# Kernel optimization log

Hardware: AMD Instinct MI355X
Metric: run time of the kernel (lower is better)

The kernel has to match this reference:

```python
import jax, jax.numpy as jnp
import numpy as np

# NOTE: ffn(in, out, capacity=1, activation) is assumed to be a single Linear(in, out)
# followed by the activation (ReLU). Dropout is identity in eval mode.

B, M, H, Eh = 16, 128, 256, 128

def setup_inputs() -> dict:
    key = jax.random.key(0)
    ks = jax.random.split(key, 12)
    s = lambda n: 1.0 / np.sqrt(n)
    return {
        "X": jax.random.normal(ks[0], (B, M, H), jnp.float32),
        "E": jax.random.normal(ks[1], (B, M, M, Eh), jnp.float32),
        "A": jax.random.uniform(ks[2], (B, M, M), jnp.float32),
        "eps": jnp.zeros((1,), jnp.float32),
        "We": jax.random.normal(ks[3], (Eh, Eh), jnp.float32) * s(Eh),
        "be": jnp.zeros((Eh,), jnp.float32),
        "Wr": jax.random.normal(ks[4], (H + Eh, H), jnp.float32) * s(H + Eh),
        "br": jnp.zeros((H,), jnp.float32),
        "W0": jax.random.normal(ks[5], (H, H), jnp.float32) * s(H),
        "b0": jnp.zeros((H,), jnp.float32),
        "W1": jax.random.normal(ks[6], (H, H), jnp.float32) * s(H),
        "b1": jnp.zeros((H,), jnp.float32),
    }

def reference(X, E, A, eps, We, be, Wr, br, W0, b0, W1, b1):
    act = jax.nn.relu
    # edge_mapper: ffn(e, e, capacity=1) -> Linear + activation
    Em = act(jnp.einsum('bije,ef->bijf', E, We) + be)          # (b,m,m,e)
    # msg[b,j,:] = sum_i A[b,i,j] * cat(X[b,i,:], Em[b,i,j,:])
    # fused: avoids materializing the (b,m,m,h+e) intermediate
    msg_x = jnp.einsum('bij,bih->bjh', A, X)                   # (b,m,h)
    msg_e = jnp.einsum('bij,bije->bje', A, Em)                 # (b,m,e)
    msg = jnp.concatenate([msg_x, msg_e], axis=-1)             # (b,m,h+e)
    Xs = (1.0 + eps) * X
    out = Xs + act(jnp.einsum('bmc,ch->bmh', msg, Wr) + br)    # residual_mapping
    out = jnp.einsum('bmh,hk->bmk', out, W0) + b0
    out = act(out)  # dropout p is identity in eval mode
    out = jnp.einsum('bmh,hk->bmk', out, W1) + b1
    out = act(out)
    return out
```

## Files before the change

### kernel.cpp

```cpp
#include <hip/hip_runtime.h>

typedef float        f32x4  __attribute__((ext_vector_type(4)));
typedef __bf16       bf16x8 __attribute__((ext_vector_type(8)));
typedef unsigned int u32x4  __attribute__((ext_vector_type(4)));
typedef unsigned short u16;

#define MFMA16(a,b,c) __builtin_amdgcn_mfma_f32_16x16x32_bf16((a),(b),(c),0,0,0)

typedef __attribute__((address_space(3))) unsigned int       as3_u32;
typedef __attribute__((address_space(1))) const unsigned int as1_u32;
__device__ __forceinline__ void gld16(const float* g, float* l) {
    __builtin_amdgcn_global_load_lds((as1_u32*)g, (as3_u32*)l, 16, 0, 0);
}

__device__ __forceinline__ unsigned bf_rnd(float x) {
    unsigned u = __float_as_uint(x);
    return (u + 0x7FFFu + ((u >> 16) & 1u)) & 0xFFFF0000u;
}
__device__ __forceinline__ void split_bf(float x, unsigned &h, unsigned &l) {
    unsigned hr = bf_rnd(x);
    h = hr >> 16;
    float lo = x - __uint_as_float(hr);
    l = bf_rnd(lo) >> 16;
}
__device__ __forceinline__ void split8q(const f32x4 a, const f32x4 b, bf16x8 &hv, bf16x8 &lv) {
    u32x4 hp, lp;
    #pragma unroll
    for (int i = 0; i < 2; ++i) {
        float x0 = (i ? b : a)[0], x1 = (i ? b : a)[1], x2 = (i ? b : a)[2], x3 = (i ? b : a)[3];
        unsigned h0 = __float_as_uint(x0) & 0xFFFF0000u;
        unsigned h1 = __float_as_uint(x1) & 0xFFFF0000u;
        unsigned h2 = __float_as_uint(x2) & 0xFFFF0000u;
        unsigned h3 = __float_as_uint(x3) & 0xFFFF0000u;
        unsigned l0 = bf_rnd(x0 - __uint_as_float(h0));
        unsigned l1 = bf_rnd(x1 - __uint_as_float(h1));
        unsigned l2 = bf_rnd(x2 - __uint_as_float(h2));
        unsigned l3 = bf_rnd(x3 - __uint_as_float(h3));
        hp[i*2+0] = (h0 >> 16) | h1;  lp[i*2+0] = (l0 >> 16) | l1;
        hp[i*2+1] = (h2 >> 16) | h3;  lp[i*2+1] = (l2 >> 16) | l3;
    }
    hv = __builtin_bit_cast(bf16x8, hp);
    lv = __builtin_bit_cast(bf16x8, lp);
}
__device__ __forceinline__ bf16x8 ld16(const u16* p) {
    return __builtin_bit_cast(bf16x8, *(const u32x4*)p);
}

__global__ __launch_bounds__(256) void k_prep(
    const float* __restrict__ We, const float* __restrict__ Wr,
    const float* __restrict__ W0, const float* __restrict__ W1,
    u16* __restrict__ WeTh, u16* __restrict__ WeTl,
    u16* __restrict__ WrTh, u16* __restrict__ WrTl,
    u16* __restrict__ W0Th, u16* __restrict__ W0Tl,
    u16* __restrict__ W1Th, u16* __restrict__ W1Tl)
{
    int t = blockIdx.x * 256 + threadIdx.x;
    float v; u16 *dh, *dl; int dst;
    if (t < 16384) {
        int f = t & 127, e = t >> 7;
        v = We[e*128 + f];
        int F = ((f>>6)*4 + ((f>>4)&3))*4 + (e>>5);
        dst = F*512 + (((e>>3)&3)*16 + (f&15))*8 + (e&7);
        dh = WeTh; dl = WeTl;
    } else if (t < 114688) {
        int u = t - 16384; int h = u & 255, k = u >> 8;
        v = Wr[k*256 + h];
        int F = (h>>4)*12 + (k>>5);
        dst = F*512 + (((k>>3)&3)*16 + (h&15))*8 + (k&7);
        dh = WrTh; dl = WrTl;
    } else if (t < 180224) {
        int u = t - 114688; int h = u & 255, k = u >> 8;
        v = W0[k*256 + h];
        int F = (h>>4)*8 + (k>>5);
        dst = F*512 + (((k>>3)&3)*16 + (h&15))*8 + (k&7);
        dh = W0Th; dl = W0Tl;
    } else {
        int u = t - 180224; int h = u & 255, k = u >> 8;
        v = W1[k*256 + h];
        int F = (h>>4)*8 + (k>>5);
        dst = F*512 + (((k>>3)&3)*16 + (h&15))*8 + (k&7);
        dh = W1Th; dl = W1Tl;
    }
    unsigned hh, ll; split_bf(v, hh, ll);
    dh[dst] = (u16)hh; dl[dst] = (u16)ll;
}

__device__ __forceinline__ void stage_slab(const float* __restrict__ Eslab,
                                           float* buf, int tid) {
    const int w = tid >> 6, l = tid & 63;
    #pragma unroll
    for (int r = 0; r < 4; ++r) {
        const int q   = (r << 2) + w;
        const int row = (q << 1) + (l >> 5);
        const int c   = ((l & 31) ^ (row & 7)) << 2;
        gld16(Eslab + row*128 + c, buf + (q << 8));
    }
}

__global__ __launch_bounds__(256) __attribute__((amdgpu_waves_per_eu(2, 2)))
void k_edge(
    const float* __restrict__ E, const float* __restrict__ A,
    const u16* __restrict__ WeTh, const u16* __restrict__ WeTl,
    const float* __restrict__ be, float* __restrict__ part)
{
    __shared__ __align__(16) float sEf[4*4096];
    __shared__ __align__(16) float sA[512];

    const int tid  = threadIdx.x;
    const int lane = tid & 63;
    const int wv   = tid >> 6;
    const int lrow = lane & 15;
    const int lk   = lane >> 4;
    const int wm   = (wv >> 1) << 4;
    const int wn   = (wv & 1)  << 6;
    const int bid  = blockIdx.x;
    const int jh   = bid & 3;
    const int c    = (bid >> 2) & 7;
    const int b    = bid >> 5;
    const int i0   = c << 4;
    const int j0   = jh << 5;

    #pragma unroll
    for (int q = 0; q < 2; ++q) {
        const int idx = q*256 + tid;
        sA[idx] = A[(size_t)(b*128 + i0 + (idx >> 5))*128 + j0 + (idx & 31)];
    }
    float ber[4];
    #pragma unroll
    for (int n = 0; n < 4; ++n) ber[n] = be[wn + n*16 + lrow];

    bf16x8 wh[4][4], wl[4][4];
    {
        const int F0 = (wv & 1) * 16;
        #pragma unroll
        for (int n = 0; n < 4; ++n)
            #pragma unroll
            for (int k = 0; k < 4; ++k) {
                const int off = (F0 + n*4 + k)*512 + lane*8;
                wh[n][k] = ld16(WeTh + off);
                wl[n][k] = ld16(WeTl + off);
            }
    }
    asm volatile("s_waitcnt vmcnt(0) lgkmcnt(0)" ::: "memory");

    const float* Eb = E + ((size_t)((b*128 + i0)*128 + j0)) * 128;
    stage_slab(Eb,            sEf,          tid);
    stage_slab(Eb + 16384,    sEf + 4096,   tid);
    stage_slab(Eb + 2*16384,  sEf + 2*4096, tid);

    f32x4 P[4] = {};

#define EDGE_STEP(S, NWs)                                                    \
    {                                                                        \
        asm volatile("s_waitcnt vmcnt(" NWs ")" ::: "memory");               \
        __builtin_amdgcn_s_barrier();                                        \
        __builtin_amdgcn_sched_barrier(0);                                   \
        if ((S) < 13)                                                        \
            stage_slab(Eb + (size_t)((S)+3)*16384,                           \
                       sEf + (((S)+3) & 3)*4096, tid);                       \
        const char* buf = (const char*)(sEf + ((S) & 3)*4096);               \
        const int jr = wm + lrow;                                            \
        const int sw = (jr & 7) << 4;                                        \
        f32x4 em[4] = {};                                                    \
        _Pragma("unroll")                                                    \
        for (int k = 0; k < 4; ++k) {                                        \
            const int cb = k*128 + lk*32;                                    \
            const f32x4 e0 = *(const f32x4*)(buf + jr*512 + ((cb +  0)^sw)); \
            const f32x4 e1 = *(const f32x4*)(buf + jr*512 + ((cb + 16)^sw)); \
            bf16x8 eh, el; split8q(e0, e1, eh, el);                          \
            _Pragma("unroll")                                                \
            for (int n = 0; n < 4; ++n) {                                    \
                em[n] = MFMA16(eh, wh[n][k], em[n]);                         \
                em[n] = MFMA16(eh, wl[n][k], em[n]);                         \
                em[n] = MFMA16(el, wh[n][k], em[n]);                         \
            }                                                                \
        }                                                                    \
        const f32x4 a4 = *(const f32x4*)(sA + (S)*32 + wm + lk*4);           \
        _Pragma("unroll")                                                    \
        for (int n = 0; n < 4; ++n)                                          \
            _Pragma("unroll")                                                \
            for (int r = 0; r < 4; ++r) {                                    \
                float v = fmaxf(em[n][r] + ber[n], 0.0f);                    \
                P[n][r] += a4[r] * v;                                        \
            }                                                                \
    }

    EDGE_STEP(0,  "8")  EDGE_STEP(1,  "8")  EDGE_STEP(2,  "8")
    EDGE_STEP(3,  "8")  EDGE_STEP(4,  "8")  EDGE_STEP(5,  "8")
    EDGE_STEP(6,  "8")  EDGE_STEP(7,  "8")  EDGE_STEP(8,  "8")
    EDGE_STEP(9,  "8")  EDGE_STEP(10, "8")  EDGE_STEP(11, "8")
    EDGE_STEP(12, "8")  EDGE_STEP(13, "8")  EDGE_STEP(14, "4")
    EDGE_STEP(15, "0")
#undef EDGE_STEP

    float* op = part + (size_t)bid * 4096;
    #pragma unroll
    for (int r = 0; r < 4; ++r) {
        const int j = wm + lk*4 + r;
        #pragma unroll
        for (int n = 0; n < 4; ++n)
            op[j*128 + wn + n*16 + lrow] = P[n][r];
    }
}

__global__ __launch_bounds__(256) void k_msg(
    const float* __restrict__ A, const float* __restrict__ X,
    const float* __restrict__ part,
    u16* __restrict__ msg_h, u16* __restrict__ msg_l)
{
    const int bid = blockIdx.x;
    const int tid = threadIdx.x;
    __shared__ float sAt[128*8];

    if (bid < 256) {
        const int b = bid >> 4, jt = bid & 15;
        #pragma unroll
        for (int q = 0; q < 4; ++q) {
            const int e   = (q << 8) + tid;
            const int row = jt*8 + (e >> 7);
            const int f   = e & 127;
            const float* p = part + ((size_t)b*32 + (row >> 5))*4096
                                  + (row & 31)*128 + f;
            float ssum = 0.f;
            #pragma unroll
            for (int cc = 0; cc < 8; ++cc) ssum += p[(size_t)cc*16384];
            unsigned hh, ll; split_bf(ssum, hh, ll);
            const size_t o = (size_t)(b*128 + row)*384 + 256 + f;
            msg_h[o] = (u16)hh; msg_l[o] = (u16)ll;
        }
    } else {
        const int idx = bid - 256;
        const int b = idx >> 4, jt = idx & 15, j0 = jt << 3;
        #pragma unroll
        for (int q = 0; q < 4; ++q) {
            const int e = tid + q*256;
            sAt[e] = A[(size_t)(b*128 + (e >> 3))*128 + j0 + (e & 7)];
        }
        __syncthreads();
        const int h = tid;
        float acc[8] = {};
        const float* Xb = X + (size_t)b*32768 + h;
        #pragma unroll 2
        for (int i = 0; i < 128; ++i) {
            const float x  = Xb[(size_t)i*256];
            const f32x4 a0 = *(const f32x4*)(sAt + i*8);
            const f32x4 a1 = *(const f32x4*)(sAt + i*8 + 4);
            acc[0] += a0[0]*x; acc[1] += a0[1]*x; acc[2] += a0[2]*x; acc[3] += a0[3]*x;
            acc[4] += a1[0]*x; acc[5] += a1[1]*x; acc[6] += a1[2]*x; acc[7] += a1[3]*x;
        }
        #pragma unroll
        for (int jj = 0; jj < 8; ++jj) {
            unsigned hh, ll; split_bf(acc[jj], hh, ll);
            const size_t o = (size_t)(b*128 + j0 + jj)*384 + h;
            msg_h[o] = (u16)hh; msg_l[o] = (u16)ll;
        }
    }
}

template<int KT, bool RES, bool F32OUT>
__global__ __launch_bounds__(256) void k_tail(
    const u16* __restrict__ Ah, const u16* __restrict__ Al,
    const u16* __restrict__ Bh, const u16* __restrict__ Bl,
    const float* __restrict__ bias, const float* __restrict__ res,
    const float* __restrict__ epsp,
    float* __restrict__ outf, u16* __restrict__ oh, u16* __restrict__ ol)
{
    constexpr int NB = KT/32;
    const int tid  = threadIdx.x;
    const int lane = tid & 63;
    const int wid  = tid >> 6;
    const int lrow = lane & 15;
    const int lk   = lane >> 4;
    const int wm   = (wid >> 1) << 4;
    const int wn   = (wid & 1)  << 5;
    const int r0   = blockIdx.x << 5;
    const int h0   = blockIdx.y << 6;

    const int arow = r0 + wm + lrow;
    const u16* pah = Ah + (size_t)arow*KT + lk*8;
    const u16* pal = Al + (size_t)arow*KT + lk*8;
    const size_t bb = (size_t)((h0 + wn) >> 4) * NB * 512 + lane*8;
    const u16* pbh = Bh + bb;
    const u16* pbl = Bl + bb;

    f32x4 P[2] = {};
    #pragma unroll
    for (int ks = 0; ks < NB; ++ks) {
        const bf16x8 ah  = ld16(pah + ks*32);
        const bf16x8 al  = ld16(pal + ks*32);
        const bf16x8 b0h = ld16(pbh + ks*512), b0l = ld16(pbl + ks*512);
        const bf16x8 b1h = ld16(pbh + (NB + ks)*512), b1l = ld16(pbl + (NB + ks)*512);
        P[0] = MFMA16(ah, b0h, P[0]);
        P[0] = MFMA16(ah, b0l, P[0]);
        P[0] = MFMA16(al, b0h, P[0]);
        P[1] = MFMA16(ah, b1h, P[1]);
        P[1] = MFMA16(ah, b1l, P[1]);
        P[1] = MFMA16(al, b1h, P[1]);
    }

    const float eps = RES ? epsp[0] : 0.f;
    #pragma unroll
    for (int n = 0; n < 2; ++n) {
        const int col = h0 + wn + n*16 + lrow;
        const float bv = bias[col];
        #pragma unroll
        for (int e = 0; e < 4; ++e) {
            const int r = r0 + wm + lk*4 + e;
            float v = fmaxf(P[n][e] + bv, 0.f);
            if (RES) v += (1.f + eps) * res[(size_t)r*256 + col];
            if (F32OUT) {
                outf[(size_t)r*256 + col] = v;
            } else {
                unsigned hh, ll; split_bf(v, hh, ll);
                oh[(size_t)r*256 + col] = (u16)hh;
                ol[(size_t)r*256 + col] = (u16)ll;
            }
        }
    }
}

extern "C" void kernel_launch(void* const* d_in, const int* in_sizes, int n_in,
                              void* d_out, int out_size, void* d_ws, size_t ws_size,
                              hipStream_t stream)
{
    const float* X   = (const float*)d_in[0];
    const float* E   = (const float*)d_in[1];
    const float* A   = (const float*)d_in[2];
    const float* eps = (const float*)d_in[3];
    const float* We  = (const float*)d_in[4];
    const float* be  = (const float*)d_in[5];
    const float* Wr  = (const float*)d_in[6];
    const float* br  = (const float*)d_in[7];
    const float* W0  = (const float*)d_in[8];
    const float* b0  = (const float*)d_in[9];
    const float* W1  = (const float*)d_in[10];
    const float* b1  = (const float*)d_in[11];
    float* out = (float*)d_out;

    u16* w = (u16*)d_ws;
    u16* WeTh = w;              u16* WeTl = WeTh + 16384;
    u16* WrTh = WeTl + 16384;   u16* WrTl = WrTh + 98304;
    u16* W0Th = WrTl + 98304;   u16* W0Tl = W0Th + 65536;
    u16* W1Th = W0Tl + 65536;   u16* W1Tl = W1Th + 65536;
    u16* msg_h = W1Tl + 65536;  u16* msg_l = msg_h + 786432;
    u16* o1h = msg_l + 786432;  u16* o1l = o1h + 524288;
    u16* o2h = o1l + 524288;    u16* o2l = o2h + 524288;
    float* part = (float*)(o2l + 524288);

    k_prep<<<960, 256, 0, stream>>>(We, Wr, W0, W1,
        WeTh, WeTl, WrTh, WrTl, W0Th, W0Tl, W1Th, W1Tl);
    k_edge<<<512, 256, 0, stream>>>(E, A, WeTh, WeTl, be, part);
    k_msg<<<512, 256, 0, stream>>>(A, X, part, msg_h, msg_l);
    k_tail<384, true , false><<<dim3(64,4), 256, 0, stream>>>(
        msg_h, msg_l, WrTh, WrTl, br, X, eps, nullptr, o1h, o1l);
    k_tail<256, false, false><<<dim3(64,4), 256, 0, stream>>>(
        o1h, o1l, W0Th, W0Tl, b0, nullptr, nullptr, nullptr, o2h, o2l);
    k_tail<256, false, true ><<<dim3(64,4), 256, 0, stream>>>(
        o2h, o2l, W1Th, W1Tl, b1, nullptr, nullptr, out, nullptr, nullptr);
}
```

Baseline: 267.4 us.

## Load edge tiles directly into registers with double buffering, drop LDS staging

The edge kernel no longer stages E slabs through LDS using global_load_lds with barriers. Each lane now loads its own E fragments and A values straight into registers, double-buffered across steps. The block grows to 512 threads with 8 waves, each covering 32 output features, and the grid halves so each block handles 32 i-rows instead of 16. The We prep layout and the partial reduction in k_msg change to match. The aim is to remove LDS traffic and barrier stalls, at the cost of uncoalesced per-lane global loads and higher register pressure.

```diff
diff --git a/kernel.cpp b/kernel.cpp
--- a/kernel.cpp
+++ b/kernel.cpp
@@ -6,12 +6,6 @@
 typedef unsigned short u16;
 
 #define MFMA16(a,b,c) __builtin_amdgcn_mfma_f32_16x16x32_bf16((a),(b),(c),0,0,0)
-
-typedef __attribute__((address_space(3))) unsigned int       as3_u32;
-typedef __attribute__((address_space(1))) const unsigned int as1_u32;
-__device__ __forceinline__ void gld16(const float* g, float* l) {
-    __builtin_amdgcn_global_load_lds((as1_u32*)g, (as3_u32*)l, 16, 0, 0);
-}
 
 __device__ __forceinline__ unsigned bf_rnd(float x) {
     unsigned u = __float_as_uint(x);
@@ -59,7 +53,7 @@
     if (t < 16384) {
         int f = t & 127, e = t >> 7;
         v = We[e*128 + f];
-        int F = ((f>>6)*4 + ((f>>4)&3))*4 + (e>>5);
+        int F = (f>>4)*4 + (e>>5);
         dst = F*512 + (((e>>3)&3)*16 + (f&15))*8 + (e&7);
         dh = WeTh; dl = WeTl;
     } else if (t < 114688) {
@@ -85,120 +79,96 @@
     dh[dst] = (u16)hh; dl[dst] = (u16)ll;
 }
 
-__device__ __forceinline__ void stage_slab(const float* __restrict__ Eslab,
-                                           float* buf, int tid) {
-    const int w = tid >> 6, l = tid & 63;
-    #pragma unroll
-    for (int r = 0; r < 4; ++r) {
-        const int q   = (r << 2) + w;
-        const int row = (q << 1) + (l >> 5);
-        const int c   = ((l & 31) ^ (row & 7)) << 2;
-        gld16(Eslab + row*128 + c, buf + (q << 8));
-    }
-}
-
-__global__ __launch_bounds__(256) __attribute__((amdgpu_waves_per_eu(2, 2)))
+__global__ __launch_bounds__(512) __attribute__((amdgpu_waves_per_eu(2, 2)))
 void k_edge(
     const float* __restrict__ E, const float* __restrict__ A,
     const u16* __restrict__ WeTh, const u16* __restrict__ WeTl,
     const float* __restrict__ be, float* __restrict__ part)
 {
-    __shared__ __align__(16) float sEf[4*4096];
-    __shared__ __align__(16) float sA[512];
-
     const int tid  = threadIdx.x;
     const int lane = tid & 63;
     const int wv   = tid >> 6;
     const int lrow = lane & 15;
     const int lk   = lane >> 4;
-    const int wm   = (wv >> 1) << 4;
-    const int wn   = (wv & 1)  << 6;
+    const int jg   = wv >> 2;
+    const int fg   = wv & 3;
+    const int wm   = jg << 4;
+    const int wn   = fg << 5;
     const int bid  = blockIdx.x;
-    const int jh   = bid & 3;
-    const int c    = (bid >> 2) & 7;
-    const int b    = bid >> 5;
-    const int i0   = c << 4;
+    const int c    = bid & 3;
+    const int jh   = (bid >> 2) & 3;
+    const int b    = bid >> 4;
+    const int i0   = c << 5;
     const int j0   = jh << 5;
 
-    #pragma unroll
-    for (int q = 0; q < 2; ++q) {
-        const int idx = q*256 + tid;
-        sA[idx] = A[(size_t)(b*128 + i0 + (idx >> 5))*128 + j0 + (idx & 31)];
-    }
-    float ber[4];
-    #pragma unroll
-    for (int n = 0; n < 4; ++n) ber[n] = be[wn + n*16 + lrow];
-
-    bf16x8 wh[4][4], wl[4][4];
-    {
-        const int F0 = (wv & 1) * 16;
-        #pragma unroll
-        for (int n = 0; n < 4; ++n)
-            #pragma unroll
-            for (int k = 0; k < 4; ++k) {
-                const int off = (F0 + n*4 + k)*512 + lane*8;
-                wh[n][k] = ld16(WeTh + off);
-                wl[n][k] = ld16(WeTl + off);
-            }
-    }
-    asm volatile("s_waitcnt vmcnt(0) lgkmcnt(0)" ::: "memory");
-
-    const float* Eb = E + ((size_t)((b*128 + i0)*128 + j0)) * 128;
-    stage_slab(Eb,            sEf,          tid);
-    stage_slab(Eb + 16384,    sEf + 4096,   tid);
-    stage_slab(Eb + 2*16384,  sEf + 2*4096, tid);
-
-    f32x4 P[4] = {};
-
-#define EDGE_STEP(S, NWs)                                                    \
-    {                                                                        \
-        asm volatile("s_waitcnt vmcnt(" NWs ")" ::: "memory");               \
-        __builtin_amdgcn_s_barrier();                                        \
-        __builtin_amdgcn_sched_barrier(0);                                   \
-        if ((S) < 13)                                                        \
-            stage_slab(Eb + (size_t)((S)+3)*16384,                           \
-                       sEf + (((S)+3) & 3)*4096, tid);                       \
-        const char* buf = (const char*)(sEf + ((S) & 3)*4096);               \
-        const int jr = wm + lrow;                                            \
-        const int sw = (jr & 7) << 4;                                        \
-        f32x4 em[4] = {};                                                    \
-        _Pragma("unroll")                                                    \
-        for (int k = 0; k < 4; ++k) {                                        \
-            const int cb = k*128 + lk*32;                                    \
-            const f32x4 e0 = *(const f32x4*)(buf + jr*512 + ((cb +  0)^sw)); \
-            const f32x4 e1 = *(const f32x4*)(buf + jr*512 + ((cb + 16)^sw)); \
-            bf16x8 eh, el; split8q(e0, e1, eh, el);                          \
-            _Pragma("unroll")                                                \
-            for (int n = 0; n < 4; ++n) {                                    \
-                em[n] = MFMA16(eh, wh[n][k], em[n]);                         \
-                em[n] = MFMA16(eh, wl[n][k], em[n]);                         \
-                em[n] = MFMA16(el, wh[n][k], em[n]);                         \
-            }                                                                \
-        }                                                                    \
-        const f32x4 a4 = *(const f32x4*)(sA + (S)*32 + wm + lk*4);           \
-        _Pragma("unroll")                                                    \
-        for (int n = 0; n < 4; ++n)                                          \
-            _Pragma("unroll")                                                \
-            for (int r = 0; r < 4; ++r) {                                    \
-                float v = fmaxf(em[n][r] + ber[n], 0.0f);                    \
-                P[n][r] += a4[r] * v;                                        \
-            }                                                                \
-    }
-
-    EDGE_STEP(0,  "8")  EDGE_STEP(1,  "8")  EDGE_STEP(2,  "8")
-    EDGE_STEP(3,  "8")  EDGE_STEP(4,  "8")  EDGE_STEP(5,  "8")
-    EDGE_STEP(6,  "8")  EDGE_STEP(7,  "8")  EDGE_STEP(8,  "8")
-    EDGE_STEP(9,  "8")  EDGE_STEP(10, "8")  EDGE_STEP(11, "8")
-    EDGE_STEP(12, "8")  EDGE_STEP(13, "8")  EDGE_STEP(14, "4")
-    EDGE_STEP(15, "0")
-#undef EDGE_STEP
+    bf16x8 wh[2][4], wl[2][4];
+    #pragma unroll
+    for (int n = 0; n < 2; ++n)
+        #pragma unroll
+        for (int k = 0; k < 4; ++k) {
+            const int off = (((fg*2 + n)*4) + k)*512 + lane*8;
+            wh[n][k] = ld16(WeTh + off);
+            wl[n][k] = ld16(WeTl + off);
+        }
+    float ber[2];
+    #pragma unroll
+    for (int n = 0; n < 2; ++n) ber[n] = be[wn + n*16 + lrow];
+
+    const float* Erow = E + ((size_t)(b*128 + i0)*128 + j0 + wm + lrow)*128 + lk*8;
+    const float* Arow = A + ((size_t)(b*128 + i0))*128 + j0 + wm + lk*4;
+
+#define LOADSLAB(dst, adst, s)                                          \
+    {                                                                   \
+        const float* p = Erow + (size_t)(s)*16384;                      \
+        _Pragma("unroll")                                               \
+        for (int k = 0; k < 4; ++k) {                                   \
+            dst[k*2+0] = *(const f32x4*)(p + k*32);                     \
+            dst[k*2+1] = *(const f32x4*)(p + k*32 + 4);                 \
+        }                                                               \
+        adst = *(const f32x4*)(Arow + (size_t)(s)*128);                 \
+    }
+
+    f32x4 ebA[8], ebB[8], a4A, a4B;
+    LOADSLAB(ebA, a4A, 0)
+
+    f32x4 P[2] = {};
+
+#define STEP(EBC, AC, EBN, AN, s)                                       \
+    {                                                                   \
+        if ((s) < 31) LOADSLAB(EBN, AN, (s)+1)                          \
+        f32x4 em0 = {}, em1 = {};                                       \
+        _Pragma("unroll")                                               \
+        for (int k = 0; k < 4; ++k) {                                   \
+            bf16x8 eh, el; split8q(EBC[k*2], EBC[k*2+1], eh, el);       \
+            em0 = MFMA16(eh, wh[0][k], em0);                            \
+            em0 = MFMA16(eh, wl[0][k], em0);                            \
+            em0 = MFMA16(el, wh[0][k], em0);                            \
+            em1 = MFMA16(eh, wh[1][k], em1);                            \
+            em1 = MFMA16(eh, wl[1][k], em1);                            \
+            em1 = MFMA16(el, wh[1][k], em1);                            \
+        }                                                               \
+        _Pragma("unroll")                                               \
+        for (int r = 0; r < 4; ++r) {                                   \
+            float v0 = fmaxf(em0[r] + ber[0], 0.0f);                    \
+            float v1 = fmaxf(em1[r] + ber[1], 0.0f);                    \
+            P[0][r] += AC[r] * v0;                                      \
+            P[1][r] += AC[r] * v1;                                      \
+        }                                                               \
+    }
+
+    for (int s = 0; s < 32; s += 2) {
+        STEP(ebA, a4A, ebB, a4B, s)
+        STEP(ebB, a4B, ebA, a4A, s+1)
+    }
+#undef STEP
+#undef LOADSLAB
 
     float* op = part + (size_t)bid * 4096;
     #pragma unroll
     for (int r = 0; r < 4; ++r) {
         const int j = wm + lk*4 + r;
         #pragma unroll
-        for (int n = 0; n < 4; ++n)
+        for (int n = 0; n < 2; ++n)
             op[j*128 + wn + n*16 + lrow] = P[n][r];
     }
 }
@@ -219,11 +189,11 @@
             const int e   = (q << 8) + tid;
             const int row = jt*8 + (e >> 7);
             const int f   = e & 127;
-            const float* p = part + ((size_t)b*32 + (row >> 5))*4096
+            const float* p = part + ((size_t)(b*16 + (row >> 5)*4))*4096
                                   + (row & 31)*128 + f;
             float ssum = 0.f;
             #pragma unroll
-            for (int cc = 0; cc < 8; ++cc) ssum += p[(size_t)cc*16384];
+            for (int cc = 0; cc < 4; ++cc) ssum += p[(size_t)cc*4096];
             unsigned hh, ll; split_bf(ssum, hh, ll);
             const size_t o = (size_t)(b*128 + row)*384 + 256 + f;
             msg_h[o] = (u16)hh; msg_l[o] = (u16)ll;
@@ -349,7 +319,7 @@
 
     k_prep<<<960, 256, 0, stream>>>(We, Wr, W0, W1,
         WeTh, WeTl, WrTh, WrTl, W0Th, W0Tl, W1Th, W1Tl);
-    k_edge<<<512, 256, 0, stream>>>(E, A, WeTh, WeTl, be, part);
+    k_edge<<<256, 512, 0, stream>>>(E, A, WeTh, WeTl, be, part);
     k_msg<<<512, 256, 0, stream>>>(A, X, part, msg_h, msg_l);
     k_tail<384, true , false><<<dim3(64,4), 256, 0, stream>>>(
         msg_h, msg_l, WrTh, WrTl, br, X, eps, nullptr, o1h, o1l);
```

Measured after the change: 294.4 us. 1.1x slower.
